# Kernel tuning notes

Measured on AMD Instinct MI355X. Metric: run time of the kernel, lower is better.

Reference implementation:

```python
import jax, jax.numpy as jnp
import numpy as np

N_NODES = 50000
N_EDGES = 600000
IN_CH = 128
HID_CH = 128
OUT_CH = 64
DEMO = 8
N_GRAPHS = 100


def setup_inputs() -> dict:
    key = jax.random.key(0)
    ks = jax.random.split(key, 16)
    s = 0.02
    inp = {
        "x": jax.random.normal(ks[0], (N_NODES, IN_CH), jnp.float32),
        "edge_index": jax.random.randint(ks[1], (2, N_EDGES), 0, N_NODES, jnp.int32),
        "batch": jnp.sort(jax.random.randint(ks[2], (N_NODES,), 0, N_GRAPHS, jnp.int32)),
        "demographic": jax.random.normal(ks[3], (N_GRAPHS, DEMO), jnp.float32),
        "W1": jax.random.normal(ks[4], (IN_CH, HID_CH), jnp.float32) * s,
        "b1": jnp.zeros((HID_CH,), jnp.float32),
        "W2": jax.random.normal(ks[5], (HID_CH, HID_CH), jnp.float32) * s,
        "b2": jnp.zeros((HID_CH,), jnp.float32),
        "W3": jax.random.normal(ks[6], (HID_CH, OUT_CH), jnp.float32) * s,
        "b3": jnp.zeros((OUT_CH,), jnp.float32),
        "Wf1": jax.random.normal(ks[7], (OUT_CH + DEMO, 64), jnp.float32) * s,
        "bf1": jnp.zeros((64,), jnp.float32),
        "Wf2": jax.random.normal(ks[8], (64, 32), jnp.float32) * s,
        "bf2": jnp.zeros((32,), jnp.float32),
        "Wf3": jax.random.normal(ks[9], (32, 2), jnp.float32) * s,
        "bf3": jnp.zeros((2,), jnp.float32),
    }
    return inp


def _gcn_conv(x, W, b, src, dst, norm, n_nodes):
    # PyG GCNConv: out_i = sum_j norm_ij * (x_j @ W) + b  (self-loops included in src/dst)
    h = x @ W
    msg = h[src] * norm[:, None]
    return jax.ops.segment_sum(msg, dst, num_segments=n_nodes) + b


def reference(x, edge_index, batch, demographic, W1, b1, W2, b2, W3, b3, Wf1, bf1, Wf2, bf2, Wf3, bf3):
    n = x.shape[0]
    # add self-loops
    loop = jnp.arange(n, dtype=edge_index.dtype)
    src = jnp.concatenate([edge_index[0], loop])
    dst = jnp.concatenate([edge_index[1], loop])
    # symmetric degree normalization: deg^{-1/2}[src] * deg^{-1/2}[dst]
    deg = jax.ops.segment_sum(jnp.ones_like(src, jnp.float32), dst, num_segments=n)
    dinv = jnp.where(deg > 0, jax.lax.rsqrt(deg), 0.0)
    norm = dinv[src] * dinv[dst]

    h = jax.nn.relu(_gcn_conv(x, W1, b1, src, dst, norm, n))
    h = jax.nn.relu(_gcn_conv(h, W2, b2, src, dst, norm, n))
    h = jax.nn.relu(_gcn_conv(h, W3, b3, src, dst, norm, n))

    # global mean pool over graphs
    g = demographic.shape[0]
    sums = jax.ops.segment_sum(h, batch, num_segments=g)
    cnts = jax.ops.segment_sum(jnp.ones((n,), jnp.float32), batch, num_segments=g)
    pooled = sums / jnp.maximum(cnts, 1.0)[:, None]

    z = jnp.concatenate([pooled, demographic], axis=1)
    z = jax.nn.relu(z @ Wf1 + bf1)
    z = jax.nn.relu(z @ Wf2 + bf2)
    return z @ Wf3 + bf3
```

## Files before the change

### kernel.cpp

```cpp
#include <hip/hip_runtime.h>


typedef __bf16 bf16x8 __attribute__((ext_vector_type(8)));
typedef float f32x4 __attribute__((ext_vector_type(4)));
typedef float f32x2 __attribute__((ext_vector_type(2)));

__device__ __forceinline__ unsigned char f32_to_fp8(float v) {
    return (unsigned char)(__builtin_amdgcn_cvt_pk_fp8_f32(v, 0.f, 0, false) & 0xff);
}
__device__ __forceinline__ void acc8_fp8(float* a, uint2 u) {
    f32x2 v;
    v = __builtin_amdgcn_cvt_pk_f32_fp8(u.x, false); a[0] += v.x; a[1] += v.y;
    v = __builtin_amdgcn_cvt_pk_f32_fp8(u.x, true);  a[2] += v.x; a[3] += v.y;
    v = __builtin_amdgcn_cvt_pk_f32_fp8(u.y, false); a[4] += v.x; a[5] += v.y;
    v = __builtin_amdgcn_cvt_pk_f32_fp8(u.y, true);  a[6] += v.x; a[7] += v.y;
}

union BF2 {
    __bf16 h[2];
    unsigned u;
};

#define PAD(c) (((c) + 15) & ~15)
#define BCAP 64
#define ECHUNK 4096
#define ECAP 4096
#define BUCKCAP 4096

__device__ __forceinline__ void wpack_block(const float* __restrict__ W,
                                            __bf16* __restrict__ hi,
                                            __bf16* __restrict__ lo, int N, int b, int l) {
    int t = b >> 2, c = b & 3;
    int k0 = c * 32 + (l >> 4) * 8;
    int ncol = t * 16 + (l & 15);
    size_t base = ((size_t)b * 64 + l) * 8;
#pragma unroll
    for (int j = 0; j < 8; j++) {
        float v = W[(size_t)(k0 + j) * N + ncol];
        __bf16 h = (__bf16)v;
        hi[base + j] = h;
        lo[base + j] = (__bf16)(v - (float)h);
    }
}

__global__ __launch_bounds__(1024) void k_bin(const int* __restrict__ src,
                                              const int* __restrict__ dst,
                                              int2* __restrict__ binbuf,
                                              int* __restrict__ bcnt,
                                              const int* __restrict__ batch,
                                              int* __restrict__ gstart,
                                              const float* __restrict__ W1,
                                              const float* __restrict__ W2,
                                              const float* __restrict__ W3,
                                              __bf16* __restrict__ Wp1h, __bf16* __restrict__ Wp1l,
                                              __bf16* __restrict__ Wp2h, __bf16* __restrict__ Wp2l,
                                              __bf16* __restrict__ Wp3h, __bf16* __restrict__ Wp3l,
                                              int E, int EC, int nbuck, int n, int G) {
    int b = blockIdx.x;
    int tid = threadIdx.x;
    if (b < EC) {
        __shared__ int lcur[512];
        for (int i = tid; i < nbuck; i += 1024) lcur[i] = 0;
        __syncthreads();
        int e0 = b * ECHUNK;
        int cntE = E - e0;
        if (cntE > ECHUNK) cntE = ECHUNK;
#pragma unroll
        for (int k = 0; k < 4; k++) {
            int idx = tid + k * 1024;
            if (idx < cntE) {
                int s = src[e0 + idx];
                int d = dst[e0 + idx];
                int bk = d >> 7;
                int slot = atomicAdd(&lcur[bk], 1);
                if (slot < BCAP) {
                    int2 sd = {s, d};
                    binbuf[((size_t)b * nbuck + bk) * BCAP + slot] = sd;
                }
            }
        }
        __syncthreads();
        for (int bk = tid; bk < nbuck; bk += 1024) {
            int c = lcur[bk];
            bcnt[b * nbuck + bk] = (c < BCAP) ? c : BCAP;
        }
        return;
    }
    if (b == EC) {
        int g = tid;
        if (g <= G) {
            int lo = 0, hi = n;
            while (lo < hi) {
                int mid = (lo + hi) >> 1;
                if (batch[mid] < g) lo = mid + 1; else hi = mid;
            }
            gstart[g] = lo;
        }
        return;
    }
    int b64 = (b - EC - 1) * 16 + (tid >> 6);
    int l = tid & 63;
    if (b64 < 32) wpack_block(W1, Wp1h, Wp1l, 128, b64, l);
    else if (b64 < 64) wpack_block(W2, Wp2h, Wp2l, 128, b64 - 32, l);
    else if (b64 < 80) wpack_block(W3, Wp3h, Wp3l, 64, b64 - 64, l);
}

__global__ __launch_bounds__(1024) void k_csr(const int2* __restrict__ binbuf,
                                              const int* __restrict__ bcnt,
                                              float* __restrict__ dinv,
                                              int2* __restrict__ rowspan,
                                              int* __restrict__ col,
                                              unsigned int* __restrict__ tzA,
                                              unsigned int* __restrict__ tzB,
                                              unsigned int* __restrict__ tz64,
                                              int n, int EC, int nbuck) {
    __shared__ int lcnt[160];
    __shared__ int lpre[161];
    __shared__ int deg[128];
    __shared__ int lloc[129];
    __shared__ int lfill[128];
    __shared__ int sedge[ECAP];
    __shared__ unsigned char redge[ECAP];
    __shared__ int cols_s[BUCKCAP];
    int b = blockIdx.x;
    int tid = threadIdx.x;
    int lane = tid & 63;
    int wid = tid >> 6;
    int r0 = b << 7;
    int r1 = r0 + 128;
    if (r1 > n) r1 = n;
    int nrows = r1 - r0;
    if (b == 0) {
        if (tid < 32) tzA[(size_t)n * 32 + tid] = 0u;
        else if (tid < 64) tzB[(size_t)n * 32 + (tid - 32)] = 0u;
        else if (tid < 80) tz64[(size_t)n * 16 + (tid - 64)] = 0u;
    }
    for (int c = tid; c < EC; c += 1024) lcnt[c] = bcnt[c * nbuck + b];
    if (tid < 128) deg[tid] = 0;
    __syncthreads();
    if (wid == 0) {
        int carry = 0;
        for (int bb = 0; bb < EC; bb += 64) {
            int idx = bb + lane;
            int val = (idx < EC) ? lcnt[idx] : 0;
            int sc = val;
#pragma unroll
            for (int d = 1; d < 64; d <<= 1) {
                int o = __shfl_up(sc, d);
                if (lane >= d) sc += o;
            }
            int grp = __shfl(sc, 63);
            if (idx < EC) lpre[idx] = sc - val + carry;
            carry += grp;
        }
        if (lane == 0) lpre[EC] = carry;
    }
    __syncthreads();
    int T = lpre[EC];
    for (int i = tid; i < T; i += 1024) {
        int lo = 0, hi = EC;
        while (lo < hi) {
            int mid = (lo + hi) >> 1;
            if (lpre[mid + 1] <= i) lo = mid + 1; else hi = mid;
        }
        int j = i - lpre[lo];
        int2 sd = binbuf[((size_t)lo * nbuck + b) * BCAP + j];
        unsigned r = (unsigned)(sd.y - r0);
        bool ok = r < (unsigned)nrows;
        if (ok) atomicAdd(&deg[r], 1);
        if (i < ECAP) {
            sedge[i] = sd.x;
            redge[i] = ok ? (unsigned char)r : (unsigned char)255;
        }
    }
    __syncthreads();
    if (wid == 0) {
        int carry = 0;
#pragma unroll
        for (int bb = 0; bb < 128; bb += 64) {
            int idx = bb + lane;
            int val = (idx < nrows) ? PAD(deg[idx]) : 0;
            int sc = val;
#pragma unroll
            for (int d = 1; d < 64; d <<= 1) {
                int o = __shfl_up(sc, d);
                if (lane >= d) sc += o;
            }
            int grp = __shfl(sc, 63);
            lloc[idx] = sc - val + carry;
            carry += grp;
        }
        if (lane == 0) lloc[128] = carry;
    }
    __syncthreads();
    int base = b * BUCKCAP;
    int tot = lloc[128];
    if (tot > BUCKCAP) tot = BUCKCAP;
    if (tid < nrows) {
        int d = deg[tid];
        lfill[tid] = lloc[tid];
        dinv[r0 + tid] = rsqrtf((float)(d + 1));
        int st = base + lloc[tid];
        int2 sp = {st, st + d};
        rowspan[r0 + tid] = sp;
    }
    for (int i = tid; i < tot; i += 1024) cols_s[i] = n;
    __syncthreads();
    int Tc = (T < ECAP) ? T : ECAP;
    for (int i = tid; i < Tc; i += 1024) {
        int r = redge[i];
        if (r != 255) {
            int pos = atomicAdd(&lfill[r], 1);
            if (pos < BUCKCAP) cols_s[pos] = sedge[i];
        }
    }
    for (int i = ECAP + tid; i < T; i += 1024) {
        int lo = 0, hi = EC;
        while (lo < hi) {
            int mid = (lo + hi) >> 1;
            if (lpre[mid + 1] <= i) lo = mid + 1; else hi = mid;
        }
        int j = i - lpre[lo];
        int2 sd = binbuf[((size_t)lo * nbuck + b) * BCAP + j];
        unsigned r = (unsigned)(sd.y - r0);
        if (r < (unsigned)nrows) {
            int pos = atomicAdd(&lfill[r], 1);
            if (pos < BUCKCAP) cols_s[pos] = sd.x;
        }
    }
    __syncthreads();
    for (int i = tid; i < tot; i += 1024) col[base + i] = cols_s[i];
}

__global__ __launch_bounds__(256) void k_gemm1(const float* __restrict__ A,
                                               const __bf16* __restrict__ Wp_hi,
                                               const __bf16* __restrict__ Wp_lo,
                                               const float* __restrict__ dinv,
                                               unsigned char* __restrict__ Cf8, int n) {
    constexpr int NT = 8;
    constexpr int N = NT * 16;
    int wave = (int)((blockIdx.x * 256u + threadIdx.x) >> 6);
    int lane = threadIdx.x & 63;
    int row0 = wave * 16;
    if (row0 >= n) return;
    int m = lane & 15;
    int q = lane >> 4;
    int row = row0 + m;
    if (row >= n) row = n - 1;
    const float* ap = A + (size_t)row * 128 + q * 8;
    bf16x8 ahi[4], alo[4];
#pragma unroll
    for (int c = 0; c < 4; c++) {
        float4 v0 = *(const float4*)(ap + c * 32);
        float4 v1 = *(const float4*)(ap + c * 32 + 4);
        float vv[8] = {v0.x, v0.y, v0.z, v0.w, v1.x, v1.y, v1.z, v1.w};
#pragma unroll
        for (int j = 0; j < 8; j++) {
            __bf16 h = (__bf16)vv[j];
            ahi[c][j] = h;
            alo[c][j] = (__bf16)(vv[j] - (float)h);
        }
    }
    float dscale[4];
#pragma unroll
    for (int r = 0; r < 4; r++) {
        int rr = row0 + q * 4 + r;
        dscale[r] = dinv[rr < n ? rr : (n - 1)];
    }
#pragma unroll
    for (int t = 0; t < NT; t++) {
        f32x4 acc = {0.f, 0.f, 0.f, 0.f};
#pragma unroll
        for (int c = 0; c < 4; c++) {
            size_t off = ((size_t)(t * 4 + c) * 64 + lane) * 8;
            bf16x8 bh = *(const bf16x8*)(Wp_hi + off);
            bf16x8 bl = *(const bf16x8*)(Wp_lo + off);
            acc = __builtin_amdgcn_mfma_f32_16x16x32_bf16(ahi[c], bh, acc, 0, 0, 0);
            acc = __builtin_amdgcn_mfma_f32_16x16x32_bf16(alo[c], bh, acc, 0, 0, 0);
            acc = __builtin_amdgcn_mfma_f32_16x16x32_bf16(ahi[c], bl, acc, 0, 0, 0);
        }
        int colx = t * 16 + m;
#pragma unroll
        for (int r = 0; r < 4; r++) {
            int orow = row0 + q * 4 + r;
            if (orow < n) Cf8[(size_t)orow * N + colx] = f32_to_fp8(acc[r] * dscale[r]);
        }
    }
}

template <int NT>
__global__ __launch_bounds__(256) void k_aggemm(const unsigned char* __restrict__ t8,
                                                const int2* __restrict__ rowspan,
                                                const int* __restrict__ col,
                                                const float* __restrict__ dinv,
                                                const float* __restrict__ bias,
                                                const __bf16* __restrict__ Wp_hi,
                                                const __bf16* __restrict__ Wp_lo,
                                                unsigned char* __restrict__ Cf8, int n) {
    constexpr int N = NT * 16;
    __shared__ __bf16 As[16][136];
    int row0 = blockIdx.x * 16;
    int tid = threadIdx.x;
    int lane = tid & 63;
    int v = tid >> 6;
    const uint2* t8v = (const uint2*)t8;
    int cg = lane & 15;
    int g = lane >> 4;
    float4 bb0 = *(const float4*)(bias + cg * 8);
    float4 bb1 = *(const float4*)(bias + cg * 8 + 4);
    float bv[8] = {bb0.x, bb0.y, bb0.z, bb0.w, bb1.x, bb1.y, bb1.z, bb1.w};
#pragma unroll 1
    for (int r = 0; r < 4; r++) {
        int lr = v * 4 + r;
        int w = row0 + lr;
        if (w < n) {
            float acc[8] = {0.f, 0.f, 0.f, 0.f, 0.f, 0.f, 0.f, 0.f};
            int2 rs = rowspan[w];
            int p = rs.x;
            int pend = p + ((rs.y - rs.x + 15) & ~15);
            for (; p < pend; p += 16) {
                int c0 = col[p + g];
                int c1 = col[p + 4 + g];
                int c2 = col[p + 8 + g];
                int c3 = col[p + 12 + g];
                uint2 u0 = t8v[((size_t)c0 << 4) + cg];
                uint2 u1 = t8v[((size_t)c1 << 4) + cg];
                uint2 u2 = t8v[((size_t)c2 << 4) + cg];
                uint2 u3 = t8v[((size_t)c3 << 4) + cg];
                acc8_fp8(acc, u0);
                acc8_fp8(acc, u1);
                acc8_fp8(acc, u2);
                acc8_fp8(acc, u3);
            }
#pragma unroll
            for (int j = 0; j < 8; j++) {
                acc[j] += __shfl_xor(acc[j], 16);
                acc[j] += __shfl_xor(acc[j], 32);
            }
            {
                uint2 us = t8v[((size_t)w << 4) + cg];
                float s8[8] = {0.f, 0.f, 0.f, 0.f, 0.f, 0.f, 0.f, 0.f};
                acc8_fp8(s8, us);
#pragma unroll
                for (int j = 0; j < 8; j++) acc[j] += s8[j];
            }
            float di = dinv[w];
            BF2 o[4];
#pragma unroll
            for (int j = 0; j < 4; j++) {
                o[j].h[0] = (__bf16)fmaxf(di * acc[2 * j] + bv[2 * j], 0.f);
                o[j].h[1] = (__bf16)fmaxf(di * acc[2 * j + 1] + bv[2 * j + 1], 0.f);
            }
            if (lane < 16) {
                uint4 st = {o[0].u, o[1].u, o[2].u, o[3].u};
                *(uint4*)&As[lr][cg * 8] = st;
            }
        } else if (lane < 16) {
            uint4 z = {0u, 0u, 0u, 0u};
            *(uint4*)&As[lr][cg * 8] = z;
        }
    }
    __syncthreads();
    int m = lane & 15;
    int q = lane >> 4;
    bf16x8 a[4];
#pragma unroll
    for (int c = 0; c < 4; c++) a[c] = *(const bf16x8*)&As[m][q * 8 + c * 32];
    float dscale[4];
#pragma unroll
    for (int r = 0; r < 4; r++) {
        int rr = row0 + q * 4 + r;
        dscale[r] = dinv[rr < n ? rr : (n - 1)];
    }
    constexpr int TPW = NT / 4;
#pragma unroll
    for (int tt = 0; tt < TPW; tt++) {
        int t = v * TPW + tt;
        f32x4 acc = {0.f, 0.f, 0.f, 0.f};
#pragma unroll
        for (int c = 0; c < 4; c++) {
            size_t off = ((size_t)(t * 4 + c) * 64 + lane) * 8;
            bf16x8 bh = *(const bf16x8*)(Wp_hi + off);
            bf16x8 bl = *(const bf16x8*)(Wp_lo + off);
            acc = __builtin_amdgcn_mfma_f32_16x16x32_bf16(a[c], bh, acc, 0, 0, 0);
            acc = __builtin_amdgcn_mfma_f32_16x16x32_bf16(a[c], bl, acc, 0, 0, 0);
        }
        int colx = t * 16 + m;
#pragma unroll
        for (int r = 0; r < 4; r++) {
            int orow = row0 + q * 4 + r;
            if (orow < n) Cf8[(size_t)orow * N + colx] = f32_to_fp8(acc[r] * dscale[r]);
        }
    }
}

__global__ __launch_bounds__(256) void k_agg64(const unsigned char* __restrict__ t8,
                                               const int2* __restrict__ rowspan,
                                               const int* __restrict__ col,
                                               const float* __restrict__ dinv,
                                               const float* __restrict__ bias,
                                               __bf16* __restrict__ out, int n) {
    int w = (int)((blockIdx.x * 256u + threadIdx.x) >> 6);
    int lane = threadIdx.x & 63;
    if (w >= n) return;
    const uint2* t8v = (const uint2*)t8;
    int cg = lane & 7;
    int g = lane >> 3;
    float acc[8] = {0.f, 0.f, 0.f, 0.f, 0.f, 0.f, 0.f, 0.f};
    int2 rs = rowspan[w];
    int p = rs.x;
    int pend = p + ((rs.y - rs.x + 15) & ~15);
    for (; p < pend; p += 16) {
        int c0 = col[p + g];
        int c1 = col[p + 8 + g];
        uint2 u0 = t8v[((size_t)c0 << 3) + cg];
        uint2 u1 = t8v[((size_t)c1 << 3) + cg];
        acc8_fp8(acc, u0);
        acc8_fp8(acc, u1);
    }
#pragma unroll
    for (int j = 0; j < 8; j++) {
        acc[j] += __shfl_xor(acc[j], 8);
        acc[j] += __shfl_xor(acc[j], 16);
        acc[j] += __shfl_xor(acc[j], 32);
    }
    {
        uint2 us = t8v[((size_t)w << 3) + cg];
        float s8[8] = {0.f, 0.f, 0.f, 0.f, 0.f, 0.f, 0.f, 0.f};
        acc8_fp8(s8, us);
#pragma unroll
        for (int j = 0; j < 8; j++) acc[j] += s8[j];
    }
    float di = dinv[w];
    float4 bb0 = *(const float4*)(bias + cg * 8);
    float4 bb1 = *(const float4*)(bias + cg * 8 + 4);
    float bv[8] = {bb0.x, bb0.y, bb0.z, bb0.w, bb1.x, bb1.y, bb1.z, bb1.w};
    BF2 o[4];
#pragma unroll
    for (int j = 0; j < 4; j++) {
        o[j].h[0] = (__bf16)fmaxf(di * acc[2 * j] + bv[2 * j], 0.f);
        o[j].h[1] = (__bf16)fmaxf(di * acc[2 * j + 1] + bv[2 * j + 1], 0.f);
    }
    if (lane < 8) {
        uint4 st = {o[0].u, o[1].u, o[2].u, o[3].u};
        *(uint4*)((unsigned int*)out + (size_t)w * 32 + cg * 4) = st;
    }
}

__global__ __launch_bounds__(256) void k_poolmlp(const unsigned short* __restrict__ h,
                                                 const int* __restrict__ gstart,
                                                 const float* __restrict__ demo,
                                                 const float* __restrict__ Wf1,
                                                 const float* __restrict__ bf1,
                                                 const float* __restrict__ Wf2,
                                                 const float* __restrict__ bf2,
                                                 const float* __restrict__ Wf3,
                                                 const float* __restrict__ bf3,
                                                 float* __restrict__ out, int G) {
    int g = blockIdx.x;
    int tid = threadIdx.x;
    int lane = tid & 63;
    int wv = tid >> 6;
    int s = gstart[g], e = gstart[g + 1];
    const unsigned* hu = (const unsigned*)h;
    int cg = lane & 15;
    int sub = lane >> 4;
    float acc[4] = {0.f, 0.f, 0.f, 0.f};
    for (int i = s + wv * 4 + sub; i < e; i += 16) {
        uint2 v = *(const uint2*)(hu + ((size_t)i << 5) + cg * 2);
        acc[0] += __uint_as_float(v.x << 16);
        acc[1] += __uint_as_float(v.x & 0xffff0000u);
        acc[2] += __uint_as_float(v.y << 16);
        acc[3] += __uint_as_float(v.y & 0xffff0000u);
    }
#pragma unroll
    for (int j = 0; j < 4; j++) {
        acc[j] += __shfl_xor(acc[j], 16);
        acc[j] += __shfl_xor(acc[j], 32);
    }
    __shared__ float red[4][64];
    __shared__ float zin[72];
    __shared__ float z1[64];
    __shared__ float z2[32];
    if (sub == 0) {
#pragma unroll
        for (int j = 0; j < 4; j++) red[wv][cg * 4 + j] = acc[j];
    }
    if (tid >= 64 && tid < 72) zin[tid] = demo[g * 8 + (tid - 64)];
    __syncthreads();
    if (tid < 64) {
        float v = red[0][tid] + red[1][tid] + red[2][tid] + red[3][tid];
        zin[tid] = v / fmaxf((float)(e - s), 1.0f);
    }
    __syncthreads();
    if (tid < 64) {
        float a = bf1[tid];
        for (int k = 0; k < 72; k++) a += zin[k] * Wf1[k * 64 + tid];
        z1[tid] = fmaxf(a, 0.f);
    }
    __syncthreads();
    if (tid < 32) {
        float a2 = bf2[tid];
        for (int k = 0; k < 64; k++) a2 += z1[k] * Wf2[k * 32 + tid];
        z2[tid] = fmaxf(a2, 0.f);
    }
    __syncthreads();
    if (tid < 2) {
        float a3 = bf3[tid];
        for (int k = 0; k < 32; k++) a3 += z2[k] * Wf3[k * 2 + tid];
        out[g * 2 + tid] = a3;
    }
}

extern "C" void kernel_launch(void* const* d_in, const int* in_sizes, int n_in,
                              void* d_out, int out_size, void* d_ws, size_t ws_size,
                              hipStream_t stream) {
    const float* x    = (const float*)d_in[0];
    const int*   ei   = (const int*)d_in[1];
    const int*   batch= (const int*)d_in[2];
    const float* demo = (const float*)d_in[3];
    const float* W1   = (const float*)d_in[4];
    const float* b1   = (const float*)d_in[5];
    const float* W2   = (const float*)d_in[6];
    const float* b2   = (const float*)d_in[7];
    const float* W3   = (const float*)d_in[8];
    const float* b3   = (const float*)d_in[9];
    const float* Wf1  = (const float*)d_in[10];
    const float* bf1  = (const float*)d_in[11];
    const float* Wf2  = (const float*)d_in[12];
    const float* bf2  = (const float*)d_in[13];
    const float* Wf3  = (const float*)d_in[14];
    const float* bf3  = (const float*)d_in[15];
    float* out = (float*)d_out;

    const int n = in_sizes[0] / 128;
    const int E = in_sizes[1] / 2;
    const int G = in_sizes[3] / 8;
    const int EC = (E + ECHUNK - 1) / ECHUNK;
    const int nbuck = (n + 127) / 128;

    char* ws = (char*)d_ws;
    auto alloc = [&](size_t bytes) {
        char* p = ws;
        ws += (bytes + 255) & ~(size_t)255;
        return p;
    };
    float*  dinv    = (float*)alloc((size_t)n * 4);
    int2*   rowspan = (int2*)alloc((size_t)n * 8);
    int*    col     = (int*)alloc((size_t)nbuck * BUCKCAP * 4 + 256);
    int2*   binbuf  = (int2*)alloc((size_t)EC * nbuck * BCAP * 8);
    int*    bcnt    = (int*)alloc((size_t)EC * nbuck * 4);
    unsigned char* tbf  = (unsigned char*)alloc((size_t)(n + 1) * 128);
    unsigned char* tbf2 = (unsigned char*)alloc((size_t)(n + 1) * 128);
    unsigned char* t3bf = (unsigned char*)alloc((size_t)(n + 1) * 64);
    __bf16* h3      = (__bf16*)alloc((size_t)n * 64 * 2);
    __bf16* Wp1h    = (__bf16*)alloc(128 * 128 * 2);
    __bf16* Wp1l    = (__bf16*)alloc(128 * 128 * 2);
    __bf16* Wp2h    = (__bf16*)alloc(128 * 128 * 2);
    __bf16* Wp2l    = (__bf16*)alloc(128 * 128 * 2);
    __bf16* Wp3h    = (__bf16*)alloc(128 * 64 * 2);
    __bf16* Wp3l    = (__bf16*)alloc(128 * 64 * 2);
    int*    gstart  = (int*)alloc((size_t)(G + 1) * 4);

    const int* srcv = ei;
    const int* dstv = ei + E;

    int waves = (n + 15) / 16;
    int gemm_blocks = (waves + 3) / 4;
    int fuse_blocks = waves;
    int agg_blocks = (int)(((size_t)n * 64 + 255) / 256);

    k_bin<<<EC + 1 + 5, 1024, 0, stream>>>(srcv, dstv, binbuf, bcnt, batch, gstart,
                                           W1, W2, W3, Wp1h, Wp1l, Wp2h, Wp2l,
                                           Wp3h, Wp3l, E, EC, nbuck, n, G);
    k_csr<<<nbuck, 1024, 0, stream>>>(binbuf, bcnt, dinv, rowspan, col,
                                      (unsigned int*)tbf, (unsigned int*)tbf2,
                                      (unsigned int*)t3bf, n, EC, nbuck);
    k_gemm1<<<gemm_blocks, 256, 0, stream>>>(x, Wp1h, Wp1l, dinv, tbf, n);
    k_aggemm<8><<<fuse_blocks, 256, 0, stream>>>(tbf, rowspan, col, dinv, b1,
                                                 Wp2h, Wp2l, tbf2, n);
    k_aggemm<4><<<fuse_blocks, 256, 0, stream>>>(tbf2, rowspan, col, dinv, b2,
                                                 Wp3h, Wp3l, t3bf, n);
    k_agg64<<<agg_blocks, 256, 0, stream>>>(t3bf, rowspan, col, dinv, b3, h3, n);
    k_poolmlp<<<G, 256, 0, stream>>>((const unsigned short*)h3, gstart, demo,
                                     Wf1, bf1, Wf2, bf2, Wf3, bf3, out, G);
}
```

Baseline: 216.9 us.

## Compute degrees globally and fuse CSR fill with first GEMM

Edge binning now sorts each chunk's edges by bucket in shared memory and writes them contiguously, recording each bucket's offset and count, instead of using fixed-capacity bucket slots. Degrees come from global atomics in the binning kernel. A new small kernel scans them into row spans and dinv, and the CSR column fill is merged into the same launch as the first GEMM so the two can run concurrently. The aim is to remove the degree pass from the CSR kernel and let CSR construction overlap with GEMM1. The cost is an extra memset and launch plus contended global atomics on gdeg.

```diff
diff --git a/kernel.cpp b/kernel.cpp
--- a/kernel.cpp
+++ b/kernel.cpp
@@ -22,9 +22,7 @@
 };
 
 #define PAD(c) (((c) + 15) & ~15)
-#define BCAP 64
 #define ECHUNK 4096
-#define ECAP 4096
 #define BUCKCAP 4096
 
 __device__ __forceinline__ void wpack_block(const float* __restrict__ W,
@@ -46,7 +44,8 @@
 __global__ __launch_bounds__(1024) void k_bin(const int* __restrict__ src,
                                               const int* __restrict__ dst,
                                               int2* __restrict__ binbuf,
-                                              int* __restrict__ bcnt,
+                                              int2* __restrict__ cinfo,
+                                              int* __restrict__ gdeg,
                                               const int* __restrict__ batch,
                                               int* __restrict__ gstart,
                                               const float* __restrict__ W1,
@@ -60,30 +59,59 @@
     int tid = threadIdx.x;
     if (b < EC) {
         __shared__ int lcur[512];
+        __shared__ int lpos[512];
+        __shared__ int2 sbuf[ECHUNK];
         for (int i = tid; i < nbuck; i += 1024) lcur[i] = 0;
         __syncthreads();
         int e0 = b * ECHUNK;
         int cntE = E - e0;
         if (cntE > ECHUNK) cntE = ECHUNK;
+        int ls[4], ld[4];
 #pragma unroll
         for (int k = 0; k < 4; k++) {
             int idx = tid + k * 1024;
             if (idx < cntE) {
-                int s = src[e0 + idx];
-                int d = dst[e0 + idx];
-                int bk = d >> 7;
-                int slot = atomicAdd(&lcur[bk], 1);
-                if (slot < BCAP) {
-                    int2 sd = {s, d};
-                    binbuf[((size_t)b * nbuck + bk) * BCAP + slot] = sd;
+                ls[k] = src[e0 + idx];
+                ld[k] = dst[e0 + idx];
+                atomicAdd(&lcur[ld[k] >> 7], 1);
+                atomicAdd(&gdeg[ld[k]], 1);
+            }
+        }
+        __syncthreads();
+        if (tid < 64) {
+            int carry = 0;
+            for (int bb = 0; bb < nbuck; bb += 64) {
+                int idx = bb + tid;
+                int val = (idx < nbuck) ? lcur[idx] : 0;
+                int sc = val;
+#pragma unroll
+                for (int d = 1; d < 64; d <<= 1) {
+                    int o = __shfl_up(sc, d);
+                    if (tid >= d) sc += o;
                 }
-            }
-        }
-        __syncthreads();
-        for (int bk = tid; bk < nbuck; bk += 1024) {
-            int c = lcur[bk];
-            bcnt[b * nbuck + bk] = (c < BCAP) ? c : BCAP;
-        }
+                int grp = __shfl(sc, 63);
+                if (idx < nbuck) lpos[idx] = sc - val + carry;
+                carry += grp;
+            }
+        }
+        __syncthreads();
+        for (int i = tid; i < nbuck; i += 1024) {
+            int2 oc = {lpos[i], lcur[i]};
+            cinfo[(size_t)b * nbuck + i] = oc;
+        }
+        __syncthreads();
+#pragma unroll
+        for (int k = 0; k < 4; k++) {
+            int idx = tid + k * 1024;
+            if (idx < cntE) {
+                int slot = atomicAdd(&lpos[ld[k] >> 7], 1);
+                int2 sd = {ls[k], ld[k]};
+                sbuf[slot] = sd;
+            }
+        }
+        __syncthreads();
+        for (int i = tid; i < cntE; i += 1024)
+            binbuf[(size_t)b * ECHUNK + i] = sbuf[i];
         return;
     }
     if (b == EC) {
@@ -105,142 +133,134 @@
     else if (b64 < 80) wpack_block(W3, Wp3h, Wp3l, 64, b64 - 64, l);
 }
 
-__global__ __launch_bounds__(1024) void k_csr(const int2* __restrict__ binbuf,
-                                              const int* __restrict__ bcnt,
-                                              float* __restrict__ dinv,
-                                              int2* __restrict__ rowspan,
-                                              int* __restrict__ col,
-                                              unsigned int* __restrict__ tzA,
-                                              unsigned int* __restrict__ tzB,
-                                              unsigned int* __restrict__ tz64,
-                                              int n, int EC, int nbuck) {
-    __shared__ int lcnt[160];
-    __shared__ int lpre[161];
-    __shared__ int deg[128];
-    __shared__ int lloc[129];
-    __shared__ int lfill[128];
-    __shared__ int sedge[ECAP];
-    __shared__ unsigned char redge[ECAP];
-    __shared__ int cols_s[BUCKCAP];
+__global__ __launch_bounds__(64) void k_span(const int* __restrict__ gdeg,
+                                             float* __restrict__ dinv,
+                                             int2* __restrict__ rowspan,
+                                             unsigned int* __restrict__ tzA,
+                                             unsigned int* __restrict__ tzB,
+                                             unsigned int* __restrict__ tz64,
+                                             int n, int nbuck) {
     int b = blockIdx.x;
-    int tid = threadIdx.x;
-    int lane = tid & 63;
-    int wid = tid >> 6;
+    int lane = threadIdx.x;
     int r0 = b << 7;
-    int r1 = r0 + 128;
-    if (r1 > n) r1 = n;
-    int nrows = r1 - r0;
+    int nrows = n - r0;
+    if (nrows > 128) nrows = 128;
+    int base = b * BUCKCAP;
+    int carry = 0;
+#pragma unroll
+    for (int half = 0; half < 2; half++) {
+        int idx = half * 64 + lane;
+        int d = (idx < nrows) ? gdeg[r0 + idx] : 0;
+        int pd = PAD(d);
+        int sc = pd;
+#pragma unroll
+        for (int s = 1; s < 64; s <<= 1) {
+            int o = __shfl_up(sc, s);
+            if (lane >= s) sc += o;
+        }
+        if (idx < nrows) {
+            int st = base + carry + sc - pd;
+            int2 sp = {st, st + d};
+            rowspan[r0 + idx] = sp;
+            dinv[r0 + idx] = rsqrtf((float)(d + 1));
+        }
+        carry += __shfl(sc, 63);
+    }
     if (b == 0) {
-        if (tid < 32) tzA[(size_t)n * 32 + tid] = 0u;
-        else if (tid < 64) tzB[(size_t)n * 32 + (tid - 32)] = 0u;
-        else if (tid < 80) tz64[(size_t)n * 16 + (tid - 64)] = 0u;
-    }
-    for (int c = tid; c < EC; c += 1024) lcnt[c] = bcnt[c * nbuck + b];
-    if (tid < 128) deg[tid] = 0;
-    __syncthreads();
-    if (wid == 0) {
-        int carry = 0;
-        for (int bb = 0; bb < EC; bb += 64) {
-            int idx = bb + lane;
-            int val = (idx < EC) ? lcnt[idx] : 0;
-            int sc = val;
-#pragma unroll
-            for (int d = 1; d < 64; d <<= 1) {
-                int o = __shfl_up(sc, d);
-                if (lane >= d) sc += o;
-            }
-            int grp = __shfl(sc, 63);
-            if (idx < EC) lpre[idx] = sc - val + carry;
-            carry += grp;
-        }
-        if (lane == 0) lpre[EC] = carry;
-    }
-    __syncthreads();
-    int T = lpre[EC];
-    for (int i = tid; i < T; i += 1024) {
-        int lo = 0, hi = EC;
-        while (lo < hi) {
-            int mid = (lo + hi) >> 1;
-            if (lpre[mid + 1] <= i) lo = mid + 1; else hi = mid;
-        }
-        int j = i - lpre[lo];
-        int2 sd = binbuf[((size_t)lo * nbuck + b) * BCAP + j];
-        unsigned r = (unsigned)(sd.y - r0);
-        bool ok = r < (unsigned)nrows;
-        if (ok) atomicAdd(&deg[r], 1);
-        if (i < ECAP) {
-            sedge[i] = sd.x;
-            redge[i] = ok ? (unsigned char)r : (unsigned char)255;
-        }
-    }
-    __syncthreads();
-    if (wid == 0) {
-        int carry = 0;
-#pragma unroll
-        for (int bb = 0; bb < 128; bb += 64) {
-            int idx = bb + lane;
-            int val = (idx < nrows) ? PAD(deg[idx]) : 0;
-            int sc = val;
-#pragma unroll
-            for (int d = 1; d < 64; d <<= 1) {
-                int o = __shfl_up(sc, d);
-                if (lane >= d) sc += o;
-            }
-            int grp = __shfl(sc, 63);
-            lloc[idx] = sc - val + carry;
-            carry += grp;
-        }
-        if (lane == 0) lloc[128] = carry;
-    }
-    __syncthreads();
-    int base = b * BUCKCAP;
-    int tot = lloc[128];
-    if (tot > BUCKCAP) tot = BUCKCAP;
-    if (tid < nrows) {
-        int d = deg[tid];
-        lfill[tid] = lloc[tid];
-        dinv[r0 + tid] = rsqrtf((float)(d + 1));
-        int st = base + lloc[tid];
-        int2 sp = {st, st + d};
-        rowspan[r0 + tid] = sp;
-    }
-    for (int i = tid; i < tot; i += 1024) cols_s[i] = n;
-    __syncthreads();
-    int Tc = (T < ECAP) ? T : ECAP;
-    for (int i = tid; i < Tc; i += 1024) {
-        int r = redge[i];
-        if (r != 255) {
-            int pos = atomicAdd(&lfill[r], 1);
-            if (pos < BUCKCAP) cols_s[pos] = sedge[i];
-        }
-    }
-    for (int i = ECAP + tid; i < T; i += 1024) {
-        int lo = 0, hi = EC;
-        while (lo < hi) {
-            int mid = (lo + hi) >> 1;
-            if (lpre[mid + 1] <= i) lo = mid + 1; else hi = mid;
-        }
-        int j = i - lpre[lo];
-        int2 sd = binbuf[((size_t)lo * nbuck + b) * BCAP + j];
-        unsigned r = (unsigned)(sd.y - r0);
-        if (r < (unsigned)nrows) {
-            int pos = atomicAdd(&lfill[r], 1);
-            if (pos < BUCKCAP) cols_s[pos] = sd.x;
-        }
-    }
-    __syncthreads();
-    for (int i = tid; i < tot; i += 1024) col[base + i] = cols_s[i];
-}
-
-__global__ __launch_bounds__(256) void k_gemm1(const float* __restrict__ A,
+        for (int i = lane; i < 80; i += 64) {
+            if (i < 32) tzA[(size_t)n * 32 + i] = 0u;
+            else if (i < 64) tzB[(size_t)n * 32 + (i - 32)] = 0u;
+            else tz64[(size_t)n * 16 + (i - 64)] = 0u;
+        }
+    }
+}
+
+__global__ __launch_bounds__(1024) void k_csrg(const int2* __restrict__ binbuf,
+                                               const int2* __restrict__ cinfo,
+                                               const int2* __restrict__ rowspan,
+                                               int* __restrict__ col,
+                                               int n, int EC, int nbuck,
+                                               const float* __restrict__ A,
                                                const __bf16* __restrict__ Wp_hi,
                                                const __bf16* __restrict__ Wp_lo,
                                                const float* __restrict__ dinv,
-                                               unsigned char* __restrict__ Cf8, int n) {
+                                               unsigned char* __restrict__ Cf8) {
+    int b = blockIdx.x;
+    int tid = threadIdx.x;
+    if (b < nbuck) {
+        __shared__ int lcnt[160];
+        __shared__ int loff[160];
+        __shared__ int lpre[161];
+        __shared__ int lfill[128];
+        __shared__ int cols_s[BUCKCAP];
+        __shared__ int stot;
+        int lane = tid & 63;
+        int wid = tid >> 6;
+        int r0 = b << 7;
+        int nrows = n - r0;
+        if (nrows > 128) nrows = 128;
+        int base = b * BUCKCAP;
+        for (int c = tid; c < EC; c += 1024) {
+            int2 oc = cinfo[(size_t)c * nbuck + b];
+            loff[c] = oc.x;
+            lcnt[c] = oc.y;
+        }
+        __syncthreads();
+        if (wid == 0) {
+            int carry = 0;
+            for (int bb = 0; bb < EC; bb += 64) {
+                int idx = bb + lane;
+                int val = (idx < EC) ? lcnt[idx] : 0;
+                int sc = val;
+#pragma unroll
+                for (int d = 1; d < 64; d <<= 1) {
+                    int o = __shfl_up(sc, d);
+                    if (lane >= d) sc += o;
+                }
+                int grp = __shfl(sc, 63);
+                if (idx < EC) lpre[idx] = sc - val + carry;
+                carry += grp;
+            }
+            if (lane == 0) lpre[EC] = carry;
+        } else if (wid == 1) {
+#pragma unroll
+            for (int half = 0; half < 2; half++) {
+                int idx = half * 64 + lane;
+                if (idx < nrows) lfill[idx] = rowspan[r0 + idx].x;
+            }
+            if (lane == 0) {
+                int2 last = rowspan[r0 + nrows - 1];
+                stot = (last.x - base) + PAD(last.y - last.x);
+            }
+        }
+        __syncthreads();
+        int T = lpre[EC];
+        int tot = stot;
+        if (tot > BUCKCAP) tot = BUCKCAP;
+        for (int i = tid; i < tot; i += 1024) cols_s[i] = n;
+        __syncthreads();
+        for (int i = tid; i < T; i += 1024) {
+            int lo = 0, hi = EC;
+            while (lo < hi) {
+                int mid = (lo + hi) >> 1;
+                if (lpre[mid + 1] <= i) lo = mid + 1; else hi = mid;
+            }
+            int j = i - lpre[lo];
+            int2 sd = binbuf[(size_t)lo * ECHUNK + loff[lo] + j];
+            unsigned r = (unsigned)(sd.y - r0);
+            if (r < (unsigned)nrows) {
+                int pos = atomicAdd(&lfill[r], 1) - base;
+                if ((unsigned)pos < (unsigned)BUCKCAP) cols_s[pos] = sd.x;
+            }
+        }
+        __syncthreads();
+        for (int i = tid; i < tot; i += 1024) col[base + i] = cols_s[i];
+        return;
+    }
     constexpr int NT = 8;
     constexpr int N = NT * 16;
-    int wave = (int)((blockIdx.x * 256u + threadIdx.x) >> 6);
-    int lane = threadIdx.x & 63;
+    int wave = (b - nbuck) * 16 + (tid >> 6);
+    int lane = tid & 63;
     int row0 = wave * 16;
     if (row0 >= n) return;
     int m = lane & 15;
@@ -547,9 +567,10 @@
     };
     float*  dinv    = (float*)alloc((size_t)n * 4);
     int2*   rowspan = (int2*)alloc((size_t)n * 8);
+    int*    gdeg    = (int*)alloc((size_t)n * 4);
     int*    col     = (int*)alloc((size_t)nbuck * BUCKCAP * 4 + 256);
-    int2*   binbuf  = (int2*)alloc((size_t)EC * nbuck * BCAP * 8);
-    int*    bcnt    = (int*)alloc((size_t)EC * nbuck * 4);
+    int2*   binbuf  = (int2*)alloc((size_t)EC * ECHUNK * 8);
+    int2*   cinfo   = (int2*)alloc((size_t)EC * nbuck * 8);
     unsigned char* tbf  = (unsigned char*)alloc((size_t)(n + 1) * 128);
     unsigned char* tbf2 = (unsigned char*)alloc((size_t)(n + 1) * 128);
     unsigned char* t3bf = (unsigned char*)alloc((size_t)(n + 1) * 64);
@@ -566,17 +587,20 @@
     const int* dstv = ei + E;
 
     int waves = (n + 15) / 16;
-    int gemm_blocks = (waves + 3) / 4;
+    int gemm1_blocks = (waves + 15) / 16;
     int fuse_blocks = waves;
     int agg_blocks = (int)(((size_t)n * 64 + 255) / 256);
 
-    k_bin<<<EC + 1 + 5, 1024, 0, stream>>>(srcv, dstv, binbuf, bcnt, batch, gstart,
-                                           W1, W2, W3, Wp1h, Wp1l, Wp2h, Wp2l,
-                                           Wp3h, Wp3l, E, EC, nbuck, n, G);
-    k_csr<<<nbuck, 1024, 0, stream>>>(binbuf, bcnt, dinv, rowspan, col,
-                                      (unsigned int*)tbf, (unsigned int*)tbf2,
-                                      (unsigned int*)t3bf, n, EC, nbuck);
-    k_gemm1<<<gemm_blocks, 256, 0, stream>>>(x, Wp1h, Wp1l, dinv, tbf, n);
+    hipMemsetAsync(gdeg, 0, (size_t)n * 4, stream);
+    k_bin<<<EC + 1 + 5, 1024, 0, stream>>>(srcv, dstv, binbuf, cinfo, gdeg, batch,
+                                           gstart, W1, W2, W3, Wp1h, Wp1l,
+                                           Wp2h, Wp2l, Wp3h, Wp3l, E, EC, nbuck, n, G);
+    k_span<<<nbuck, 64, 0, stream>>>(gdeg, dinv, rowspan,
+                                     (unsigned int*)tbf, (unsigned int*)tbf2,
+                                     (unsigned int*)t3bf, n, nbuck);
+    k_csrg<<<nbuck + gemm1_blocks, 1024, 0, stream>>>(binbuf, cinfo, rowspan, col,
+                                                      n, EC, nbuck,
+                                                      x, Wp1h, Wp1l, dinv, tbf);
     k_aggemm<8><<<fuse_blocks, 256, 0, stream>>>(tbf, rowspan, col, dinv, b1,
                                                  Wp2h, Wp2l, tbf2, n);
     k_aggemm<4><<<fuse_blocks, 256, 0, stream>>>(tbf2, rowspan, col, dinv, b2,
```

Result: slower. 246.5 us (+13.7%).

## Compute degrees globally in binning and fuse layer-1 GEMM into CSR kernel

Applied to the files above, without the earlier changes.

Degrees are now accumulated with global atomics during edge binning, so the CSR build no longer needs a separate degree pass over binned edges. Binned edges are packed into 32-bit words (16-bit source plus a 7-bit local row) to halve binbuf traffic. The layer-1 GEMM is merged into the CSR launch as extra blocks that derive dinv straight from the global degrees, saving one kernel launch and letting GEMM overlap CSR construction. In exchange there is an extra memset and a global atomic per edge, and the 16-bit source packing only works while the node count stays below 65536.

```diff
diff --git a/kernel.cpp b/kernel.cpp
--- a/kernel.cpp
+++ b/kernel.cpp
@@ -24,7 +24,6 @@
 #define PAD(c) (((c) + 15) & ~15)
 #define BCAP 64
 #define ECHUNK 4096
-#define ECAP 4096
 #define BUCKCAP 4096
 
 __device__ __forceinline__ void wpack_block(const float* __restrict__ W,
@@ -45,8 +44,9 @@
 
 __global__ __launch_bounds__(1024) void k_bin(const int* __restrict__ src,
                                               const int* __restrict__ dst,
-                                              int2* __restrict__ binbuf,
+                                              unsigned int* __restrict__ binbuf,
                                               int* __restrict__ bcnt,
+                                              int* __restrict__ gdeg,
                                               const int* __restrict__ batch,
                                               int* __restrict__ gstart,
                                               const float* __restrict__ W1,
@@ -72,10 +72,11 @@
                 int s = src[e0 + idx];
                 int d = dst[e0 + idx];
                 int bk = d >> 7;
+                atomicAdd(&gdeg[d], 1);
                 int slot = atomicAdd(&lcur[bk], 1);
                 if (slot < BCAP) {
-                    int2 sd = {s, d};
-                    binbuf[((size_t)b * nbuck + bk) * BCAP + slot] = sd;
+                    binbuf[((size_t)b * nbuck + bk) * BCAP + slot] =
+                        (unsigned)s | ((unsigned)(d & 127) << 16);
                 }
             }
         }
@@ -105,142 +106,112 @@
     else if (b64 < 80) wpack_block(W3, Wp3h, Wp3l, 64, b64 - 64, l);
 }
 
-__global__ __launch_bounds__(1024) void k_csr(const int2* __restrict__ binbuf,
+__global__ __launch_bounds__(1024) void k_csr(const unsigned int* __restrict__ binbuf,
                                               const int* __restrict__ bcnt,
+                                              const int* __restrict__ gdeg,
                                               float* __restrict__ dinv,
                                               int2* __restrict__ rowspan,
                                               int* __restrict__ col,
                                               unsigned int* __restrict__ tzA,
                                               unsigned int* __restrict__ tzB,
                                               unsigned int* __restrict__ tz64,
-                                              int n, int EC, int nbuck) {
-    __shared__ int lcnt[160];
-    __shared__ int lpre[161];
-    __shared__ int deg[128];
-    __shared__ int lloc[129];
-    __shared__ int lfill[128];
-    __shared__ int sedge[ECAP];
-    __shared__ unsigned char redge[ECAP];
-    __shared__ int cols_s[BUCKCAP];
+                                              int n, int EC, int nbuck,
+                                              const float* __restrict__ A,
+                                              const __bf16* __restrict__ Wp_hi,
+                                              const __bf16* __restrict__ Wp_lo,
+                                              unsigned char* __restrict__ Cf8) {
     int b = blockIdx.x;
     int tid = threadIdx.x;
-    int lane = tid & 63;
-    int wid = tid >> 6;
-    int r0 = b << 7;
-    int r1 = r0 + 128;
-    if (r1 > n) r1 = n;
-    int nrows = r1 - r0;
-    if (b == 0) {
-        if (tid < 32) tzA[(size_t)n * 32 + tid] = 0u;
-        else if (tid < 64) tzB[(size_t)n * 32 + (tid - 32)] = 0u;
-        else if (tid < 80) tz64[(size_t)n * 16 + (tid - 64)] = 0u;
-    }
-    for (int c = tid; c < EC; c += 1024) lcnt[c] = bcnt[c * nbuck + b];
-    if (tid < 128) deg[tid] = 0;
-    __syncthreads();
-    if (wid == 0) {
-        int carry = 0;
-        for (int bb = 0; bb < EC; bb += 64) {
-            int idx = bb + lane;
-            int val = (idx < EC) ? lcnt[idx] : 0;
-            int sc = val;
-#pragma unroll
-            for (int d = 1; d < 64; d <<= 1) {
-                int o = __shfl_up(sc, d);
-                if (lane >= d) sc += o;
-            }
-            int grp = __shfl(sc, 63);
-            if (idx < EC) lpre[idx] = sc - val + carry;
-            carry += grp;
-        }
-        if (lane == 0) lpre[EC] = carry;
-    }
-    __syncthreads();
-    int T = lpre[EC];
-    for (int i = tid; i < T; i += 1024) {
-        int lo = 0, hi = EC;
-        while (lo < hi) {
-            int mid = (lo + hi) >> 1;
-            if (lpre[mid + 1] <= i) lo = mid + 1; else hi = mid;
-        }
-        int j = i - lpre[lo];
-        int2 sd = binbuf[((size_t)lo * nbuck + b) * BCAP + j];
-        unsigned r = (unsigned)(sd.y - r0);
-        bool ok = r < (unsigned)nrows;
-        if (ok) atomicAdd(&deg[r], 1);
-        if (i < ECAP) {
-            sedge[i] = sd.x;
-            redge[i] = ok ? (unsigned char)r : (unsigned char)255;
-        }
-    }
-    __syncthreads();
-    if (wid == 0) {
-        int carry = 0;
-#pragma unroll
-        for (int bb = 0; bb < 128; bb += 64) {
-            int idx = bb + lane;
-            int val = (idx < nrows) ? PAD(deg[idx]) : 0;
-            int sc = val;
-#pragma unroll
-            for (int d = 1; d < 64; d <<= 1) {
-                int o = __shfl_up(sc, d);
-                if (lane >= d) sc += o;
-            }
-            int grp = __shfl(sc, 63);
-            lloc[idx] = sc - val + carry;
-            carry += grp;
-        }
-        if (lane == 0) lloc[128] = carry;
-    }
-    __syncthreads();
-    int base = b * BUCKCAP;
-    int tot = lloc[128];
-    if (tot > BUCKCAP) tot = BUCKCAP;
-    if (tid < nrows) {
-        int d = deg[tid];
-        lfill[tid] = lloc[tid];
-        dinv[r0 + tid] = rsqrtf((float)(d + 1));
-        int st = base + lloc[tid];
-        int2 sp = {st, st + d};
-        rowspan[r0 + tid] = sp;
-    }
-    for (int i = tid; i < tot; i += 1024) cols_s[i] = n;
-    __syncthreads();
-    int Tc = (T < ECAP) ? T : ECAP;
-    for (int i = tid; i < Tc; i += 1024) {
-        int r = redge[i];
-        if (r != 255) {
+    if (b < nbuck) {
+        __shared__ int lcnt[160];
+        __shared__ int lpre[161];
+        __shared__ int ldeg[128];
+        __shared__ int lloc[129];
+        __shared__ int lfill[128];
+        __shared__ int cols_s[BUCKCAP];
+        int lane = tid & 63;
+        int wid = tid >> 6;
+        int r0 = b << 7;
+        int r1 = r0 + 128;
+        if (r1 > n) r1 = n;
+        int nrows = r1 - r0;
+        if (b == 0) {
+            if (tid < 32) tzA[(size_t)n * 32 + tid] = 0u;
+            else if (tid < 64) tzB[(size_t)n * 32 + (tid - 32)] = 0u;
+            else if (tid < 80) tz64[(size_t)n * 16 + (tid - 64)] = 0u;
+        }
+        for (int c = tid; c < EC; c += 1024) lcnt[c] = bcnt[c * nbuck + b];
+        if (tid < 128) ldeg[tid] = (tid < nrows) ? gdeg[r0 + tid] : 0;
+        __syncthreads();
+        if (wid == 0) {
+            int carry = 0;
+            for (int bb = 0; bb < EC; bb += 64) {
+                int idx = bb + lane;
+                int val = (idx < EC) ? lcnt[idx] : 0;
+                int sc = val;
+#pragma unroll
+                for (int d = 1; d < 64; d <<= 1) {
+                    int o = __shfl_up(sc, d);
+                    if (lane >= d) sc += o;
+                }
+                int grp = __shfl(sc, 63);
+                if (idx < EC) lpre[idx] = sc - val + carry;
+                carry += grp;
+            }
+            if (lane == 0) lpre[EC] = carry;
+        } else if (wid == 1) {
+            int carry = 0;
+#pragma unroll
+            for (int bb = 0; bb < 128; bb += 64) {
+                int idx = bb + lane;
+                int val = (idx < nrows) ? PAD(ldeg[idx]) : 0;
+                int sc = val;
+#pragma unroll
+                for (int d = 1; d < 64; d <<= 1) {
+                    int o = __shfl_up(sc, d);
+                    if (lane >= d) sc += o;
+                }
+                int grp = __shfl(sc, 63);
+                lloc[idx] = sc - val + carry;
+                carry += grp;
+            }
+            if (lane == 0) lloc[128] = carry;
+        }
+        __syncthreads();
+        int base = b * BUCKCAP;
+        int T = lpre[EC];
+        int tot = lloc[128];
+        if (tot > BUCKCAP) tot = BUCKCAP;
+        if (tid < nrows) {
+            int d = ldeg[tid];
+            lfill[tid] = lloc[tid];
+            dinv[r0 + tid] = rsqrtf((float)(d + 1));
+            int st = base + lloc[tid];
+            int2 sp = {st, st + d};
+            rowspan[r0 + tid] = sp;
+        }
+        for (int i = tid; i < tot; i += 1024) cols_s[i] = n;
+        __syncthreads();
+        for (int i = tid; i < T; i += 1024) {
+            int lo = 0, hi = EC;
+            while (lo < hi) {
+                int mid = (lo + hi) >> 1;
+                if (lpre[mid + 1] <= i) lo = mid + 1; else hi = mid;
+            }
+            int j = i - lpre[lo];
+            unsigned pk = binbuf[((size_t)lo * nbuck + b) * BCAP + j];
+            int r = (int)(pk >> 16);
             int pos = atomicAdd(&lfill[r], 1);
-            if (pos < BUCKCAP) cols_s[pos] = sedge[i];
-        }
-    }
-    for (int i = ECAP + tid; i < T; i += 1024) {
-        int lo = 0, hi = EC;
-        while (lo < hi) {
-            int mid = (lo + hi) >> 1;
-            if (lpre[mid + 1] <= i) lo = mid + 1; else hi = mid;
-        }
-        int j = i - lpre[lo];
-        int2 sd = binbuf[((size_t)lo * nbuck + b) * BCAP + j];
-        unsigned r = (unsigned)(sd.y - r0);
-        if (r < (unsigned)nrows) {
-            int pos = atomicAdd(&lfill[r], 1);
-            if (pos < BUCKCAP) cols_s[pos] = sd.x;
-        }
-    }
-    __syncthreads();
-    for (int i = tid; i < tot; i += 1024) col[base + i] = cols_s[i];
-}
-
-__global__ __launch_bounds__(256) void k_gemm1(const float* __restrict__ A,
-                                               const __bf16* __restrict__ Wp_hi,
-                                               const __bf16* __restrict__ Wp_lo,
-                                               const float* __restrict__ dinv,
-                                               unsigned char* __restrict__ Cf8, int n) {
+            if ((unsigned)pos < (unsigned)BUCKCAP) cols_s[pos] = (int)(pk & 0xffffu);
+        }
+        __syncthreads();
+        for (int i = tid; i < tot; i += 1024) col[base + i] = cols_s[i];
+        return;
+    }
     constexpr int NT = 8;
     constexpr int N = NT * 16;
-    int wave = (int)((blockIdx.x * 256u + threadIdx.x) >> 6);
-    int lane = threadIdx.x & 63;
+    int wave = (b - nbuck) * 16 + (tid >> 6);
+    int lane = tid & 63;
     int row0 = wave * 16;
     if (row0 >= n) return;
     int m = lane & 15;
@@ -265,7 +236,7 @@
 #pragma unroll
     for (int r = 0; r < 4; r++) {
         int rr = row0 + q * 4 + r;
-        dscale[r] = dinv[rr < n ? rr : (n - 1)];
+        dscale[r] = rsqrtf((float)(gdeg[rr < n ? rr : (n - 1)] + 1));
     }
 #pragma unroll
     for (int t = 0; t < NT; t++) {
@@ -547,8 +518,9 @@
     };
     float*  dinv    = (float*)alloc((size_t)n * 4);
     int2*   rowspan = (int2*)alloc((size_t)n * 8);
+    int*    gdeg    = (int*)alloc((size_t)n * 4);
     int*    col     = (int*)alloc((size_t)nbuck * BUCKCAP * 4 + 256);
-    int2*   binbuf  = (int2*)alloc((size_t)EC * nbuck * BCAP * 8);
+    unsigned int* binbuf = (unsigned int*)alloc((size_t)EC * nbuck * BCAP * 4);
     int*    bcnt    = (int*)alloc((size_t)EC * nbuck * 4);
     unsigned char* tbf  = (unsigned char*)alloc((size_t)(n + 1) * 128);
     unsigned char* tbf2 = (unsigned char*)alloc((size_t)(n + 1) * 128);
@@ -566,17 +538,21 @@
     const int* dstv = ei + E;
 
     int waves = (n + 15) / 16;
-    int gemm_blocks = (waves + 3) / 4;
+    int gemm1_blocks = (waves + 15) / 16;
     int fuse_blocks = waves;
     int agg_blocks = (int)(((size_t)n * 64 + 255) / 256);
 
-    k_bin<<<EC + 1 + 5, 1024, 0, stream>>>(srcv, dstv, binbuf, bcnt, batch, gstart,
-                                           W1, W2, W3, Wp1h, Wp1l, Wp2h, Wp2l,
-                                           Wp3h, Wp3l, E, EC, nbuck, n, G);
-    k_csr<<<nbuck, 1024, 0, stream>>>(binbuf, bcnt, dinv, rowspan, col,
-                                      (unsigned int*)tbf, (unsigned int*)tbf2,
-                                      (unsigned int*)t3bf, n, EC, nbuck);
-    k_gemm1<<<gemm_blocks, 256, 0, stream>>>(x, Wp1h, Wp1l, dinv, tbf, n);
+    hipMemsetAsync(gdeg, 0, (size_t)n * 4, stream);
+    k_bin<<<EC + 1 + 5, 1024, 0, stream>>>(srcv, dstv, binbuf, bcnt, gdeg, batch,
+                                           gstart, W1, W2, W3, Wp1h, Wp1l,
+                                           Wp2h, Wp2l, Wp3h, Wp3l, E, EC, nbuck, n, G);
+    k_csr<<<nbuck + gemm1_blocks, 1024, 0, stream>>>(binbuf, bcnt, gdeg, dinv,
+                                                     rowspan, col,
+                                                     (unsigned int*)tbf,
+                                                     (unsigned int*)tbf2,
+                                                     (unsigned int*)t3bf,
+                                                     n, EC, nbuck,
+                                                     x, Wp1h, Wp1l, tbf);
     k_aggemm<8><<<fuse_blocks, 256, 0, stream>>>(tbf, rowspan, col, dinv, b1,
                                                  Wp2h, Wp2l, tbf2, n);
     k_aggemm<4><<<fuse_blocks, 256, 0, stream>>>(tbf2, rowspan, col, dinv, b2,
```

Result: slower. 242.0 us (+11.6%).
